# Kernel optimization log

Hardware: AMD Instinct MI355X
Metric: run time of the kernel (lower is better)

## Reference

```python
import jax, jax.numpy as jnp
import numpy as np

M = 2          # interp_dim
D = 4          # interp_degree
MESH_LOWER = np.array([0.0, 0.0], dtype=np.float32)
MESH_UPPER = np.array([1.0, 1.0], dtype=np.float32)
MESH_SIZE = np.array([64, 64], dtype=np.int32)   # coe grid = mesh_size*D+1 = [257, 257]


def _lagrange_basis(t):
    """t: [N, M] local coordinate in [0, D]; returns bases [N, M, D+1].
    L_j(t) = prod_{k != j} (t - k) / (j - k)."""
    ks = jnp.arange(D + 1, dtype=t.dtype)
    tk = t[..., None] - ks                       # [N, M, D+1]
    bs = []
    for j in range(D + 1):                       # small fixed loop over D+1=5 bases
        num = jnp.ones(t.shape, t.dtype)
        denom = 1.0
        for k in range(D + 1):
            if k != j:
                num = num * tk[..., k]
                denom *= float(j - k)
        bs.append(num / denom)
    return jnp.stack(bs, axis=-1)                # [N, M, D+1]


def setup_inputs() -> dict:
    key = jax.random.key(0)
    k1, k2 = jax.random.split(key)
    inputs = jax.random.uniform(k1, (2048, 2048, M), dtype=jnp.float32)  # points in [0,1)^2
    grid = tuple(int(s) * D + 1 for s in MESH_SIZE)                      # (257, 257)
    interp_coe = jax.random.normal(k2, grid, dtype=jnp.float32)
    return {"inputs": inputs, "interp_coe": interp_coe}


def reference(inputs, interp_coe):
    size = inputs.shape
    x = inputs.reshape(-1, M)                                   # [N, M]
    lower = jnp.asarray(MESH_LOWER, x.dtype)
    upper = jnp.asarray(MESH_UPPER, x.dtype)
    msize = jnp.asarray(MESH_SIZE.astype(np.float32), x.dtype)
    u = (x - lower) / (upper - lower) * msize                   # grid coordinates
    cell = jnp.clip(jnp.floor(u), 0.0, msize - 1.0)             # [N, M] element index
    t = (u - cell) * D                                          # local coord in [0, D]
    basis = _lagrange_basis(t)                                  # [N, M, D+1]
    base = cell.astype(jnp.int32) * D                           # [N, M] global node base index
    offs = jnp.arange(D + 1, dtype=jnp.int32)
    i0 = base[:, 0, None] + offs                                # [N, D+1]
    i1 = base[:, 1, None] + offs                                # [N, D+1]
    coe = interp_coe[i0[:, :, None], i1[:, None, :]]            # [N, D+1, D+1] gathered cell coes
    out = jnp.einsum('nij,ni,nj->n', coe, basis[:, 0], basis[:, 1])
    return out.reshape(size[:-1])
```

## Files before the change

kernel.cpp:

```cpp
#include <hip/hip_runtime.h>

#define NGRID 257
#define LDS_PITCH 260
#define LDS_BYTES (LDS_PITCH * NGRID * 2)
#define BLOCK 1024
#define GRID 128
#define OUTER 16

typedef _Float16 half2_t __attribute__((ext_vector_type(2)));
typedef _Float16 half4_t __attribute__((ext_vector_type(4)));
typedef float    f32x2  __attribute__((ext_vector_type(2)));

struct __attribute__((packed, aligned(4))) f4u { float x, y, z, w; };

__device__ __forceinline__ half2_t pack2(float a, float b) {
    return __builtin_bit_cast(half2_t, __builtin_amdgcn_cvt_pkrtz(a, b));
}

__device__ __forceinline__ float rowscale(int r) {
    return (r & 1) ? (-1.0f / 6.0f) : ((r & 2) ? 0.25f : (1.0f / 24.0f));
}

__device__ __forceinline__ void nbasis(f32x2 fr, f32x2 n[5]) {
    f32x2 f0 = fr * 4.0f;
    f32x2 f1 = f0 - 1.0f;
    f32x2 f2 = f0 - 2.0f;
    f32x2 f3 = f1 - 2.0f;
    f32x2 f4 = f0 - 4.0f;
    f32x2 p01 = f0 * f1;
    f32x2 p12 = f1 * f2;
    f32x2 p23 = f2 * f3;
    f32x2 p34 = f3 * f4;
    n[0] = p12 * p34;
    n[1] = (f0 * f2) * p34;
    n[2] = p01 * p34;
    n[3] = p01 * (f2 * f4);
    n[4] = p01 * p23;
}

__device__ __forceinline__ float2 eval2(const _Float16* __restrict__ lds,
                                        float xa0, float xa1,
                                        float xb0, float xb1) {
    float ua0 = xa0 * 64.0f, ua1 = xa1 * 64.0f;
    float ub0 = xb0 * 64.0f, ub1 = xb1 * 64.0f;
    int ia0 = (int)ua0, ia1 = (int)ua1;
    int ib0 = (int)ub0, ib1 = (int)ub1;
    f32x2 frA = { __builtin_amdgcn_fractf(ua0), __builtin_amdgcn_fractf(ua1) };
    f32x2 frB = { __builtin_amdgcn_fractf(ub0), __builtin_amdgcn_fractf(ub1) };

    const _Float16* baseA  = lds + (ia0 * 4) * LDS_PITCH + ia1 * 4;
    const _Float16* baseA2 = baseA + 2 * LDS_PITCH;
    const _Float16* baseB  = lds + (ib0 * 4) * LDS_PITCH + ib1 * 4;
    const _Float16* baseB2 = baseB + 2 * LDS_PITCH;

    half4_t la0 = *(const half4_t*)(baseA);
    half4_t la1 = *(const half4_t*)(baseA + LDS_PITCH);
    half4_t la2 = *(const half4_t*)(baseA2);
    half4_t la3 = *(const half4_t*)(baseA2 + LDS_PITCH);
    half4_t la4 = *(const half4_t*)(baseA2 + 2 * LDS_PITCH);
    half2_t ha0 = *(const half2_t*)(baseA + 4);
    half2_t ha1 = *(const half2_t*)(baseA + LDS_PITCH + 4);
    half2_t ha2 = *(const half2_t*)(baseA2 + 4);
    half2_t ha3 = *(const half2_t*)(baseA2 + LDS_PITCH + 4);
    half2_t ha4 = *(const half2_t*)(baseA2 + 2 * LDS_PITCH + 4);

    half4_t lb0 = *(const half4_t*)(baseB);
    half4_t lb1 = *(const half4_t*)(baseB + LDS_PITCH);
    half4_t lb2 = *(const half4_t*)(baseB2);
    half4_t lb3 = *(const half4_t*)(baseB2 + LDS_PITCH);
    half4_t lb4 = *(const half4_t*)(baseB2 + 2 * LDS_PITCH);
    half2_t hb0 = *(const half2_t*)(baseB + 4);
    half2_t hb1 = *(const half2_t*)(baseB + LDS_PITCH + 4);
    half2_t hb2 = *(const half2_t*)(baseB2 + 4);
    half2_t hb3 = *(const half2_t*)(baseB2 + LDS_PITCH + 4);
    half2_t hb4 = *(const half2_t*)(baseB2 + 2 * LDS_PITCH + 4);

    f32x2 nA[5], nB[5];
    nbasis(frA, nA);
    nbasis(frB, nB);
    half2_t qA01 = pack2(nA[0][1], nA[1][1]);
    half2_t qA23 = pack2(nA[2][1], nA[3][1]);
    float   bA4  = nA[4][1];
    half2_t qB01 = pack2(nB[0][1], nB[1][1]);
    half2_t qB23 = pack2(nB[2][1], nB[3][1]);
    float   bB4  = nB[4][1];

    half4_t loA[5] = { la0, la1, la2, la3, la4 };
    half2_t hiA[5] = { ha0, ha1, ha2, ha3, ha4 };
    half4_t loB[5] = { lb0, lb1, lb2, lb3, lb4 };
    half2_t hiB[5] = { hb0, hb1, hb2, hb3, hb4 };

    float rdA[5], rdB[5];
#pragma unroll
    for (int i = 0; i < 5; ++i) {
        half2_t xy = __builtin_shufflevector(loA[i], loA[i], 0, 1);
        half2_t zw = __builtin_shufflevector(loA[i], loA[i], 2, 3);
        float r = (float)hiA[i][0] * bA4;
        r = __builtin_amdgcn_fdot2(zw, qA23, r, false);
        r = __builtin_amdgcn_fdot2(xy, qA01, r, false);
        rdA[i] = r;
    }
#pragma unroll
    for (int i = 0; i < 5; ++i) {
        half2_t xy = __builtin_shufflevector(loB[i], loB[i], 0, 1);
        half2_t zw = __builtin_shufflevector(loB[i], loB[i], 2, 3);
        float r = (float)hiB[i][0] * bB4;
        r = __builtin_amdgcn_fdot2(zw, qB23, r, false);
        r = __builtin_amdgcn_fdot2(xy, qB01, r, false);
        rdB[i] = r;
    }

    float accA = nA[4][0] * rdA[4];
    accA = fmaf(nA[0][0], rdA[0], accA);
    accA = fmaf(nA[2][0], rdA[2], accA);
    float accA2 = nA[1][0] * rdA[1];
    accA2 = fmaf(nA[3][0], rdA[3], accA2);

    float accB = nB[4][0] * rdB[4];
    accB = fmaf(nB[0][0], rdB[0], accB);
    accB = fmaf(nB[2][0], rdB[2], accB);
    float accB2 = nB[1][0] * rdB[1];
    accB2 = fmaf(nB[3][0], rdB[3], accB2);

    float2 r;
    r.x = accA + accA2;
    r.y = accB + accB2;
    return r;
}

__launch_bounds__(BLOCK, 4)
__global__ void lagrange_kernel(const float* __restrict__ inputs,
                                const float* __restrict__ coe,
                                float* __restrict__ out,
                                int npts) {
    extern __shared__ _Float16 lds[];
    const int t = threadIdx.x;

#pragma unroll
    for (int k = 0; k < 16; ++k) {
        int g = t + k * BLOCK;
        int r = g >> 6;
        int c4 = (g & 63) << 2;
        f4u q = *(const f4u*)(coe + r * NGRID + c4);
        float rs = rowscale(r);
        half4_t h = { (_Float16)(q.x * (rs * (1.0f / 24.0f))),
                      (_Float16)(q.y * (rs * (-1.0f / 6.0f))),
                      (_Float16)(q.z * (rs * 0.25f)),
                      (_Float16)(q.w * (rs * (-1.0f / 6.0f))) };
        *(half4_t*)(lds + r * LDS_PITCH + c4) = h;
    }
    if (t < 64) {
        int c4 = t << 2;
        f4u q = *(const f4u*)(coe + 256 * NGRID + c4);
        const float rs = 1.0f / 24.0f;
        half4_t h = { (_Float16)(q.x * (rs * (1.0f / 24.0f))),
                      (_Float16)(q.y * (rs * (-1.0f / 6.0f))),
                      (_Float16)(q.z * (rs * 0.25f)),
                      (_Float16)(q.w * (rs * (-1.0f / 6.0f))) };
        *(half4_t*)(lds + 256 * LDS_PITCH + c4) = h;
    }
    if (t < NGRID) {
        float rs = rowscale(t);
        lds[t * LDS_PITCH + 256] = (_Float16)(coe[t * NGRID + 256] * (rs * (1.0f / 24.0f)));
    }
    __syncthreads();

    const float2* __restrict__ in2 = (const float2*)inputs;
    const int tid = blockIdx.x * BLOCK + t;
    const int stride = GRID * BLOCK;
    (void)npts;

    float2 a0 = in2[tid];
    float2 a1 = in2[tid + stride];
    float2 a2 = in2[tid + 2 * stride];
    float2 b0 = in2[tid + OUTER * stride];
    float2 b1 = in2[tid + (OUTER + 1) * stride];
    float2 b2 = in2[tid + (OUTER + 2) * stride];
#pragma unroll
    for (int k = 0; k < OUTER; ++k) {
        float2 a3, b3;
        if (k + 3 < OUTER) {
            a3 = in2[tid + (k + 3) * stride];
            b3 = in2[tid + (k + OUTER + 3) * stride];
        }
        float2 r = eval2(lds, a0.x, a0.y, b0.x, b0.y);
        __builtin_nontemporal_store(r.x, &out[tid + k * stride]);
        __builtin_nontemporal_store(r.y, &out[tid + (k + OUTER) * stride]);
        a0 = a1; a1 = a2; a2 = a3;
        b0 = b1; b1 = b2; b2 = b3;
    }
}

extern "C" void kernel_launch(void* const* d_in, const int* in_sizes, int n_in,
                              void* d_out, int out_size, void* d_ws, size_t ws_size,
                              hipStream_t stream) {
    const float* inputs = (const float*)d_in[0];
    const float* coe    = (const float*)d_in[1];
    float* out = (float*)d_out;
    int npts = out_size;

    (void)hipFuncSetAttribute((const void*)lagrange_kernel,
                              hipFuncAttributeMaxDynamicSharedMemorySize,
                              LDS_BYTES);

    dim3 grid(GRID), block(BLOCK);
    hipLaunchKernelGGL(lagrange_kernel, grid, block, LDS_BYTES, stream,
                       inputs, coe, out, npts);
}
```

Before: 92.63 us.

## Double grid size and overlap coefficient table staging with input prefetch

Doubles the grid to 256 blocks, each handling half as many points per thread, so more blocks are available to fill the GPU. The first input points are now loaded before the LDS coefficient table is built, and all 16 coefficient loads are issued up front before any conversion and LDS store, so global memory latency overlaps. The cost is that every block rebuilds the whole fp16 table in LDS, so table-building work doubles relative to the useful work, and holding all 16 loads in flight raises register pressure.

Measured after the change: 86.04 us. 1.08x faster.

```diff
diff --git a/kernel.cpp b/kernel.cpp
--- a/kernel.cpp
+++ b/kernel.cpp
@@ -4,8 +4,8 @@
 #define LDS_PITCH 260
 #define LDS_BYTES (LDS_PITCH * NGRID * 2)
 #define BLOCK 1024
-#define GRID 128
-#define OUTER 16
+#define GRID 256
+#define OUTER 8
 
 typedef _Float16 half2_t __attribute__((ext_vector_type(2)));
 typedef _Float16 half4_t __attribute__((ext_vector_type(4)));
@@ -135,39 +135,9 @@
                                 int npts) {
     extern __shared__ _Float16 lds[];
     const int t = threadIdx.x;
-
-#pragma unroll
-    for (int k = 0; k < 16; ++k) {
-        int g = t + k * BLOCK;
-        int r = g >> 6;
-        int c4 = (g & 63) << 2;
-        f4u q = *(const f4u*)(coe + r * NGRID + c4);
-        float rs = rowscale(r);
-        half4_t h = { (_Float16)(q.x * (rs * (1.0f / 24.0f))),
-                      (_Float16)(q.y * (rs * (-1.0f / 6.0f))),
-                      (_Float16)(q.z * (rs * 0.25f)),
-                      (_Float16)(q.w * (rs * (-1.0f / 6.0f))) };
-        *(half4_t*)(lds + r * LDS_PITCH + c4) = h;
-    }
-    if (t < 64) {
-        int c4 = t << 2;
-        f4u q = *(const f4u*)(coe + 256 * NGRID + c4);
-        const float rs = 1.0f / 24.0f;
-        half4_t h = { (_Float16)(q.x * (rs * (1.0f / 24.0f))),
-                      (_Float16)(q.y * (rs * (-1.0f / 6.0f))),
-                      (_Float16)(q.z * (rs * 0.25f)),
-                      (_Float16)(q.w * (rs * (-1.0f / 6.0f))) };
-        *(half4_t*)(lds + 256 * LDS_PITCH + c4) = h;
-    }
-    if (t < NGRID) {
-        float rs = rowscale(t);
-        lds[t * LDS_PITCH + 256] = (_Float16)(coe[t * NGRID + 256] * (rs * (1.0f / 24.0f)));
-    }
-    __syncthreads();
-
-    const float2* __restrict__ in2 = (const float2*)inputs;
     const int tid = blockIdx.x * BLOCK + t;
     const int stride = GRID * BLOCK;
+    const float2* __restrict__ in2 = (const float2*)inputs;
     (void)npts;
 
     float2 a0 = in2[tid];
@@ -176,6 +146,43 @@
     float2 b0 = in2[tid + OUTER * stride];
     float2 b1 = in2[tid + (OUTER + 1) * stride];
     float2 b2 = in2[tid + (OUTER + 2) * stride];
+
+    float tail_col = 0.0f;
+    if (t < NGRID) tail_col = coe[t * NGRID + 256];
+    f4u qr;
+    if (t < 64) qr = *(const f4u*)(coe + 256 * NGRID + (t << 2));
+    f4u q[16];
+#pragma unroll
+    for (int k = 0; k < 16; ++k) {
+        int g = t + k * BLOCK;
+        q[k] = *(const f4u*)(coe + (g >> 6) * NGRID + ((g & 63) << 2));
+    }
+#pragma unroll
+    for (int k = 0; k < 16; ++k) {
+        int g = t + k * BLOCK;
+        int r = g >> 6;
+        int c4 = (g & 63) << 2;
+        float rs = rowscale(r);
+        half4_t h = { (_Float16)(q[k].x * (rs * (1.0f / 24.0f))),
+                      (_Float16)(q[k].y * (rs * (-1.0f / 6.0f))),
+                      (_Float16)(q[k].z * (rs * 0.25f)),
+                      (_Float16)(q[k].w * (rs * (-1.0f / 6.0f))) };
+        *(half4_t*)(lds + r * LDS_PITCH + c4) = h;
+    }
+    if (t < 64) {
+        const float rs = 1.0f / 24.0f;
+        half4_t h = { (_Float16)(qr.x * (rs * (1.0f / 24.0f))),
+                      (_Float16)(qr.y * (rs * (-1.0f / 6.0f))),
+                      (_Float16)(qr.z * (rs * 0.25f)),
+                      (_Float16)(qr.w * (rs * (-1.0f / 6.0f))) };
+        *(half4_t*)(lds + 256 * LDS_PITCH + (t << 2)) = h;
+    }
+    if (t < NGRID) {
+        float rs = rowscale(t);
+        lds[t * LDS_PITCH + 256] = (_Float16)(tail_col * (rs * (1.0f / 24.0f)));
+    }
+    __syncthreads();
+
 #pragma unroll
     for (int k = 0; k < OUTER; ++k) {
         float2 a3, b3;
```
